# Kernel optimization log

Measured on AMD Instinct MI355X. Metric: run time of the kernel, lower is better.

The kernel has to match this reference:

```python
import jax, jax.numpy as jnp
import numpy as np

E = 1024
H = 16
D = E // H
NUM_BUCKETS = 320
MAX_DISTANCE = 800


def _relative_positions_bucket(relative_positions):
    # relative_positions: int32 [T, S]
    num_buckets = NUM_BUCKETS // 2  # 160
    relative_buckets = (relative_positions > 0).astype(jnp.int32) * num_buckets
    rel = jnp.abs(relative_positions)
    max_exact = num_buckets // 2  # 80
    is_small = rel < max_exact
    rel_f = jnp.maximum(rel, 1).astype(jnp.float32)
    large = jnp.log(rel_f / max_exact) / np.log(MAX_DISTANCE / max_exact) * (num_buckets - max_exact)
    large = (max_exact + large).astype(jnp.int32)
    large = jnp.minimum(large, num_buckets - 1)
    relative_buckets = relative_buckets + jnp.where(is_small, rel, large)
    return relative_buckets


def setup_inputs() -> dict:
    key = jax.random.key(0)
    ks = jax.random.split(key, 12)
    B, T = 2, 2048
    s = 0.02
    return {
        "hidden_states": jax.random.normal(ks[0], (B, T, E), dtype=jnp.float32),
        "q_w": jax.random.normal(ks[1], (E, E), dtype=jnp.float32) * s,
        "q_b": jnp.zeros((E,), dtype=jnp.float32),
        "k_w": jax.random.normal(ks[2], (E, E), dtype=jnp.float32) * s,
        "k_b": jnp.zeros((E,), dtype=jnp.float32),
        "v_w": jax.random.normal(ks[3], (E, E), dtype=jnp.float32) * s,
        "v_b": jnp.zeros((E,), dtype=jnp.float32),
        "out_w": jax.random.normal(ks[4], (E, E), dtype=jnp.float32) * s,
        "out_b": jnp.zeros((E,), dtype=jnp.float32),
        "rel_embed": jax.random.normal(ks[5], (NUM_BUCKETS, H), dtype=jnp.float32) * s,
        "gru_const": jnp.ones((1, H, 1, 1), dtype=jnp.float32),
        "gru_w": jax.random.normal(ks[6], (8, D), dtype=jnp.float32) * s,
        "gru_b": jnp.zeros((8,), dtype=jnp.float32),
    }


def reference(hidden_states, q_w, q_b, k_w, k_b, v_w, v_b, out_w, out_b,
              rel_embed, gru_const, gru_w, gru_b):
    B, T, _ = hidden_states.shape
    scaling = D ** (-0.5)

    # --- relative position bias: [H, T, T] ---
    ctx = jnp.arange(T, dtype=jnp.int32)[:, None]
    mem = jnp.arange(T, dtype=jnp.int32)[None, :]
    buckets = _relative_positions_bucket(mem - ctx)          # [T, T]
    position_bias = rel_embed[buckets]                        # [T, T, H]
    position_bias = jnp.transpose(position_bias, (2, 0, 1))   # [H, T, T]

    # --- gate (gru_rel_pos): per (b, h, t) scalar ---
    gated = hidden_states.reshape(B, T, H, D).transpose(0, 2, 1, 3)  # [B,H,T,D]
    proj = jnp.einsum('bhtd,ed->bhte', gated, gru_w) + gru_b         # [B,H,T,8]
    proj = proj.reshape(B, H, T, 2, 4).sum(-1)                        # [B,H,T,2]
    gate = jax.nn.sigmoid(proj)
    gate_a = gate[..., 0:1]
    gate_b = gate[..., 1:2]
    gate_out = gate_a * (gate_b * gru_const - 1.0) + 2.0              # [B,H,T,1]
    gated_position_bias = gate_out * position_bias[None]              # [B,H,T,T]

    # --- attention (same math as F.multi_head_attention_forward eager path) ---
    q = (hidden_states @ q_w.T + q_b).reshape(B, T, H, D).transpose(0, 2, 1, 3) * scaling
    k = (hidden_states @ k_w.T + k_b).reshape(B, T, H, D).transpose(0, 2, 1, 3)
    v = (hidden_states @ v_w.T + v_b).reshape(B, T, H, D).transpose(0, 2, 1, 3)

    scores = jnp.einsum('bhtd,bhsd->bhts', q, k) + gated_position_bias
    attn = jax.nn.softmax(scores, axis=-1)
    ctx_out = jnp.einsum('bhts,bhsd->bhtd', attn, v)                  # [B,H,T,D]
    ctx_out = ctx_out.transpose(0, 2, 1, 3).reshape(B, T, E)
    return ctx_out @ out_w.T + out_b
```

## Files before the change

kernel.cpp:

```cpp
#include <hip/hip_runtime.h>
#include <hip/hip_bf16.h>
#include <math.h>

typedef __bf16 bf16;
typedef __bf16 bf16x4 __attribute__((ext_vector_type(4)));
typedef __bf16 bf16x8 __attribute__((ext_vector_type(8)));
typedef float  f32x4  __attribute__((ext_vector_type(4)));

#define T_SEQ 2048
#define E_DIM 1024
#define H_NUM 16
#define D_DIM 64
#define NDELTA 4095
#define LOG2E 1.4426950408889634f

__device__ __forceinline__ void gld16(const bf16* g, bf16* l) {
  __builtin_amdgcn_global_load_lds((__attribute__((address_space(1))) void*)(g),
                                   (__attribute__((address_space(3))) void*)(l), 16, 0, 0);
}

__global__ void cast_bf16_kernel(const float* __restrict__ src, bf16* __restrict__ dst, int n4) {
  int i = blockIdx.x * blockDim.x + threadIdx.x;
  if (i >= n4) return;
  const float4 v = reinterpret_cast<const float4*>(src)[i];
  bf16x4 o;
  o[0] = (bf16)v.x; o[1] = (bf16)v.y; o[2] = (bf16)v.z; o[3] = (bf16)v.w;
  reinterpret_cast<bf16x4*>(dst)[i] = o;
}

__global__ void cast_w_kernel(const float* __restrict__ q_w, const float* __restrict__ k_w,
                              const float* __restrict__ v_w, const float* __restrict__ o_w,
                              bf16* __restrict__ wcat, bf16* __restrict__ wob) {
  int i = blockIdx.x * 256 + threadIdx.x;
  int sel = blockIdx.y;
  const float* src = (sel == 0) ? q_w : (sel == 1) ? k_w : (sel == 2) ? v_w : o_w;
  bf16* dst = (sel < 3) ? (wcat + (size_t)sel * 1048576) : wob;
  const float4 v = reinterpret_cast<const float4*>(src)[i];
  bf16x4 o;
  o[0] = (bf16)v.x; o[1] = (bf16)v.y; o[2] = (bf16)v.z; o[3] = (bf16)v.w;
  reinterpret_cast<bf16x4*>(dst)[i] = o;
}

__global__ void pb_kernel(const float* __restrict__ rel_embed, float* __restrict__ pbt) {
  int dd = blockIdx.x * 64 + threadIdx.x;
  if (dd >= NDELTA) return;
  int delta = dd - (T_SEQ - 1);
  int bucket = (delta > 0) ? 160 : 0;
  int rel = abs(delta);
  int v;
  if (rel < 80) {
    v = rel;
  } else {
    float rf = (float)(rel < 1 ? 1 : rel);
    float lf = logf(rf / 80.0f) * (80.0f / 2.302585092994046f);
    int lg = 80 + (int)lf;
    v = lg < 159 ? lg : 159;
  }
  bucket += v;
#pragma unroll
  for (int h = 0; h < H_NUM; h++)
    pbt[h * NDELTA + dd] = rel_embed[bucket * H_NUM + h];
}

__global__ __launch_bounds__(256)
void gate_kernel(const float* __restrict__ hs, const float* __restrict__ gru_w,
                 const float* __restrict__ gru_b, const float* __restrict__ gconst,
                 float* __restrict__ gate)
{
  __shared__ float w[512];
  int tid = threadIdx.x;
  w[tid] = gru_w[tid];
  w[tid + 256] = gru_w[tid + 256];
  __syncthreads();
  int idx = blockIdx.x * 256 + tid;
  int h  = idx & 15;
  int bt = idx >> 4;
  const float* x = hs + (size_t)bt * E_DIM + h * D_DIM;
  float acc[8] = {0,0,0,0,0,0,0,0};
  for (int d = 0; d < 64; d += 4) {
    float4 xv = *(const float4*)&x[d];
#pragma unroll
    for (int e = 0; e < 8; e++) {
      acc[e] += xv.x * w[e*64+d] + xv.y * w[e*64+d+1]
              + xv.z * w[e*64+d+2] + xv.w * w[e*64+d+3];
    }
  }
  float p0 = acc[0]+acc[1]+acc[2]+acc[3] + gru_b[0]+gru_b[1]+gru_b[2]+gru_b[3];
  float p1 = acc[4]+acc[5]+acc[6]+acc[7] + gru_b[4]+gru_b[5]+gru_b[6]+gru_b[7];
  float ga = 1.0f / (1.0f + expf(-p0));
  float gb = 1.0f / (1.0f + expf(-p1));
  float g = (ga * (gb * gconst[h] - 1.0f) + 2.0f) * LOG2E;
  int bb = bt >> 11;
  int t  = bt & (T_SEQ - 1);
  gate[((size_t)(bb * H_NUM + h)) * T_SEQ + t] = g;
}

template<int MODE, int BM, int BN>
__global__ __launch_bounds__(256, 4)
void gemm4_kernel(const bf16* __restrict__ A, const bf16* __restrict__ W,
                  const float* __restrict__ b0, const float* __restrict__ b1,
                  const float* __restrict__ b2, float qalpha,
                  void* __restrict__ out0, void* __restrict__ out1, void* __restrict__ out2)
{
  constexpr int AM = BM / 32;
  constexpr int AN = BN / 32;
  __shared__ bf16 As[2][BM * 32];
  __shared__ bf16 Bs[2][BN * 32];
  const int tid  = threadIdx.x;
  const int lane = tid & 63;
  const int wave = tid >> 6;
  const int m0 = blockIdx.y * BM;
  const int n0 = blockIdx.x * BN;
  const int wm = (wave >> 1) * (BM / 2);
  const int wn = (wave & 1) * (BN / 2);
  const int qd = lane >> 4;
  const int lm = lane & 15;

  const int row4 = lane >> 2;
  const int col8 = (lane & 3) * 8;
  const bf16* gA0 = A + (size_t)(m0 + wave * (BM / 4) + row4) * 1024 + col8;
  const bf16* gB0 = W + (size_t)(n0 + wave * (BN / 4) + row4) * 1024 + col8;
  bf16* lA = (bf16*)As + wave * (BM / 4) * 32;
  bf16* lB = (bf16*)Bs + wave * (BN / 4) * 32;

  gld16(gA0, lA);
  if (BM == 128) gld16(gA0 + (size_t)16 * 1024, lA + 512);
  gld16(gB0, lB);
  if (BN == 128) gld16(gB0 + (size_t)16 * 1024, lB + 512);
  __syncthreads();

  f32x4 acc[AM][AN] = {};

  for (int k0 = 0; k0 < 1024; k0 += 32) {
    const int buf = (k0 >> 5) & 1;
    if (k0 + 32 < 1024) {
      bf16* lA1 = lA + (buf ^ 1) * (BM * 32);
      bf16* lB1 = lB + (buf ^ 1) * (BN * 32);
      gld16(gA0 + k0 + 32, lA1);
      if (BM == 128) gld16(gA0 + (size_t)16 * 1024 + k0 + 32, lA1 + 512);
      gld16(gB0 + k0 + 32, lB1);
      if (BN == 128) gld16(gB0 + (size_t)16 * 1024 + k0 + 32, lB1 + 512);
    }
    bf16x8 af[AM], bfr[AN];
#pragma unroll
    for (int i = 0; i < AM; i++)
      af[i]  = *(const bf16x8*)&As[buf][(wm + i * 16 + lm) * 32 + qd * 8];
#pragma unroll
    for (int i = 0; i < AN; i++)
      bfr[i] = *(const bf16x8*)&Bs[buf][(wn + i * 16 + lm) * 32 + qd * 8];
#pragma unroll
    for (int im = 0; im < AM; im++)
#pragma unroll
      for (int in = 0; in < AN; in++)
        acc[im][in] = __builtin_amdgcn_mfma_f32_16x16x32_bf16(af[im], bfr[in], acc[im][in], 0, 0, 0);
    __syncthreads();
  }

  const int seg = n0 >> 10;
  const float* bias = (MODE == 0) ? b0 : (seg == 0 ? b0 : (seg == 1 ? b1 : b2));
  const float alpha = (MODE == 1 && seg == 0) ? qalpha : 1.0f;

#pragma unroll
  for (int im = 0; im < AM; im++) {
#pragma unroll
    for (int in = 0; in < AN; in++) {
      const int n  = n0 + wn + in * 16 + lm;
      const int n1 = n & 1023;
      const float bv = bias[n1];
      const int mb = m0 + wm + im * 16 + qd * 4;
      if (MODE == 0) {
        float* o = (float*)out0;
#pragma unroll
        for (int r = 0; r < 4; r++)
          o[(size_t)(mb + r) * 1024 + n1] = acc[im][in][r] + bv;
      } else if (seg == 2) {
        const int bb = mb >> 11;
        const int t  = mb & 2047;
        bf16x4 pk;
#pragma unroll
        for (int r = 0; r < 4; r++) pk[r] = (bf16)(acc[im][in][r] + bv);
        *(bf16x4*)&((bf16*)out2)[((size_t)(bb * 1024 + n1)) * 2048 + t] = pk;
      } else {
        bf16* o = (bf16*)(seg == 0 ? out0 : out1);
#pragma unroll
        for (int r = 0; r < 4; r++)
          o[(size_t)(mb + r) * 1024 + n1] = (bf16)((acc[im][in][r] + bv) * alpha);
      }
    }
  }
}

#define LK 72
__global__ __launch_bounds__(256)
void attn3_kernel(const bf16* __restrict__ Qg, const bf16* __restrict__ Kg,
                  const bf16* __restrict__ Vtg, const float* __restrict__ gate,
                  const float* __restrict__ pbt, bf16* __restrict__ ctx)
{
  __shared__ bf16 Ks[2][64 * LK];
  __shared__ bf16 Vs[2][64 * LK];
  __shared__ bf16 Ps[4][32 * LK];
  __shared__ float pbs[2176];

  const int t0 = blockIdx.x * 128;
  const int h  = blockIdx.y;
  const int b  = blockIdx.z;
  const int tid  = threadIdx.x;
  const int lane = tid & 63;
  const int wave = tid >> 6;
  const int qd = lane >> 4;
  const int lm = lane & 15;

  for (int i = tid; i < 2176; i += 256) {
    int idx = i - t0 + 1920;
    pbs[i] = (idx >= 0 && idx < NDELTA) ? pbt[h * NDELTA + idx] : 0.0f;
  }

  bf16x8 qf[2][2];
  float g[2];
#pragma unroll
  for (int nb = 0; nb < 2; nb++) {
    const int q = t0 + wave * 32 + nb * 16 + lm;
    const bf16* qrow = Qg + (size_t)(b * T_SEQ + q) * E_DIM + h * D_DIM;
    qf[nb][0] = *(const bf16x8*)(qrow + qd * 8);
    qf[nb][1] = *(const bf16x8*)(qrow + 32 + qd * 8);
    g[nb] = gate[((size_t)(b * H_NUM + h)) * T_SEQ + q];
  }

  const int srow = tid >> 2;
  const int scol = (tid & 3) * 16;
  const bf16* kgp = Kg  + ((size_t)(b * T_SEQ) + srow) * E_DIM + h * D_DIM + scol;
  const bf16* vgp = Vtg + ((size_t)(b * 1024) + h * D_DIM + srow) * T_SEQ + scol;

  {
    bf16x8 a0 = *(const bf16x8*)kgp;
    bf16x8 a1 = *(const bf16x8*)(kgp + 8);
    bf16x8 c0 = *(const bf16x8*)vgp;
    bf16x8 c1 = *(const bf16x8*)(vgp + 8);
    *(bf16x8*)&Ks[0][srow * LK + scol]     = a0;
    *(bf16x8*)&Ks[0][srow * LK + scol + 8] = a1;
    *(bf16x8*)&Vs[0][srow * LK + scol]     = c0;
    *(bf16x8*)&Vs[0][srow * LK + scol + 8] = c1;
  }
  __syncthreads();

  f32x4 o[4][2] = {};
  float li[2] = {0.0f, 0.0f};
  bf16* psw = &Ps[wave][0];

  for (int it = 0; it < T_SEQ / 64; it++) {
    const int s0 = it * 64;
    const int buf = it & 1;
    const bool more = (it + 1 < T_SEQ / 64);
    bf16x8 nk0, nk1, nv0, nv1;
    if (more) {
      const bf16* kn = kgp + (size_t)(s0 + 64) * E_DIM;
      const bf16* vn = vgp + (s0 + 64);
      nk0 = *(const bf16x8*)kn; nk1 = *(const bf16x8*)(kn + 8);
      nv0 = *(const bf16x8*)vn; nv1 = *(const bf16x8*)(vn + 8);
    }

    bf16x8 kf[4][2];
#pragma unroll
    for (int mb = 0; mb < 4; mb++) {
      kf[mb][0] = *(const bf16x8*)&Ks[buf][(16 * mb + lm) * LK + qd * 8];
      kf[mb][1] = *(const bf16x8*)&Ks[buf][(16 * mb + lm) * LK + 32 + qd * 8];
    }
#pragma unroll
    for (int nb = 0; nb < 2; nb++) {
      f32x4 sc[4];
#pragma unroll
      for (int mb = 0; mb < 4; mb++) {
        f32x4 t = {};
        t = __builtin_amdgcn_mfma_f32_16x16x32_bf16(kf[mb][0], qf[nb][0], t, 0, 0, 0);
        t = __builtin_amdgcn_mfma_f32_16x16x32_bf16(kf[mb][1], qf[nb][1], t, 0, 0, 0);
        sc[mb] = t;
      }
      const int ib = s0 + 4 * qd + 127 - (wave * 32 + nb * 16 + lm);
      float rs = 0.0f;
#pragma unroll
      for (int mb = 0; mb < 4; mb++) {
        bf16x4 pk;
#pragma unroll
        for (int r = 0; r < 4; r++) {
          float p = __builtin_amdgcn_exp2f(sc[mb][r] + g[nb] * pbs[ib + 16 * mb + r]);
          rs += p;
          pk[r] = (bf16)p;
        }
        *(bf16x4*)&psw[(nb * 16 + lm) * LK + 16 * mb + 4 * qd] = pk;
      }
      li[nb] += rs;
    }
    bf16x8 pf[2][2];
#pragma unroll
    for (int nb = 0; nb < 2; nb++) {
      pf[nb][0] = *(const bf16x8*)&psw[(nb * 16 + lm) * LK + qd * 8];
      pf[nb][1] = *(const bf16x8*)&psw[(nb * 16 + lm) * LK + 32 + qd * 8];
    }
#pragma unroll
    for (int db = 0; db < 4; db++) {
      bf16x8 vf0 = *(const bf16x8*)&Vs[buf][(16 * db + lm) * LK + qd * 8];
      bf16x8 vf1 = *(const bf16x8*)&Vs[buf][(16 * db + lm) * LK + 32 + qd * 8];
#pragma unroll
      for (int nb = 0; nb < 2; nb++) {
        o[db][nb] = __builtin_amdgcn_mfma_f32_16x16x32_bf16(vf0, pf[nb][0], o[db][nb], 0, 0, 0);
        o[db][nb] = __builtin_amdgcn_mfma_f32_16x16x32_bf16(vf1, pf[nb][1], o[db][nb], 0, 0, 0);
      }
    }
    if (more) {
      *(bf16x8*)&Ks[buf ^ 1][srow * LK + scol]     = nk0;
      *(bf16x8*)&Ks[buf ^ 1][srow * LK + scol + 8] = nk1;
      *(bf16x8*)&Vs[buf ^ 1][srow * LK + scol]     = nv0;
      *(bf16x8*)&Vs[buf ^ 1][srow * LK + scol + 8] = nv1;
    }
    __syncthreads();
  }

#pragma unroll
  for (int nb = 0; nb < 2; nb++) {
    li[nb] += __shfl_xor(li[nb], 16);
    li[nb] += __shfl_xor(li[nb], 32);
  }
#pragma unroll
  for (int nb = 0; nb < 2; nb++) {
    const float inv = 1.0f / li[nb];
    const int q = t0 + wave * 32 + nb * 16 + lm;
    bf16* obase = ctx + (size_t)(b * T_SEQ + q) * E_DIM + h * D_DIM + 4 * qd;
#pragma unroll
    for (int db = 0; db < 4; db++) {
      bf16x4 ov;
      ov[0] = (bf16)(o[db][nb][0] * inv); ov[1] = (bf16)(o[db][nb][1] * inv);
      ov[2] = (bf16)(o[db][nb][2] * inv); ov[3] = (bf16)(o[db][nb][3] * inv);
      *(bf16x4*)&obase[16 * db] = ov;
    }
  }
}

extern "C" void kernel_launch(void* const* d_in, const int* in_sizes, int n_in,
                              void* d_out, int out_size, void* d_ws, size_t ws_size,
                              hipStream_t stream)
{
  const float* hs     = (const float*)d_in[0];
  const float* q_w    = (const float*)d_in[1];
  const float* q_b    = (const float*)d_in[2];
  const float* k_w    = (const float*)d_in[3];
  const float* k_b    = (const float*)d_in[4];
  const float* v_w    = (const float*)d_in[5];
  const float* v_b    = (const float*)d_in[6];
  const float* out_w  = (const float*)d_in[7];
  const float* out_b  = (const float*)d_in[8];
  const float* rel    = (const float*)d_in[9];
  const float* gconst = (const float*)d_in[10];
  const float* gru_w  = (const float*)d_in[11];
  const float* gru_b  = (const float*)d_in[12];

  char* p = (char*)d_ws;
  bf16* hsb  = (bf16*)p; p += (size_t)4096 * 1024 * 2;
  bf16* wcat = (bf16*)p; p += (size_t)3072 * 1024 * 2;
  bf16* wob  = (bf16*)p; p += (size_t)1024 * 1024 * 2;
  bf16* Qb   = (bf16*)p; p += (size_t)4096 * 1024 * 2;
  bf16* Kb   = (bf16*)p; p += (size_t)4096 * 1024 * 2;
  bf16* Vtb  = (bf16*)p; p += (size_t)2048 * 2048 * 2;
  bf16* ctxb = (bf16*)p; p += (size_t)4096 * 1024 * 2;
  float* gatep = (float*)p; p += (size_t)2 * H_NUM * T_SEQ * 4;
  float* pbt   = (float*)p; p += (size_t)H_NUM * NDELTA * 4;

  cast_bf16_kernel<<<4096, 256, 0, stream>>>(hs, hsb, 1048576);
  cast_w_kernel<<<dim3(1024, 4), 256, 0, stream>>>(q_w, k_w, v_w, out_w, wcat, wob);
  pb_kernel<<<64, 64, 0, stream>>>(rel, pbt);
  gate_kernel<<<256, 256, 0, stream>>>(hs, gru_w, gru_b, gconst, gatep);

  const float qalpha = 0.125f * LOG2E;
  gemm4_kernel<1, 64, 128><<<dim3(24, 64), 256, 0, stream>>>(
      hsb, wcat, q_b, k_b, v_b, qalpha, Qb, Kb, Vtb);

  attn3_kernel<<<dim3(T_SEQ / 128, H_NUM, 2), 256, 0, stream>>>(Qb, Kb, Vtb, gatep, pbt, ctxb);

  gemm4_kernel<0, 64, 64><<<dim3(16, 64), 256, 0, stream>>>(
      ctxb, wob, out_b, nullptr, nullptr, 1.0f, d_out, nullptr, nullptr);
}
```

Baseline: 229.9 us.

## Read position bias from four shifted bf16 copies in global memory instead of LDS

The bias table is now built as four copies per head, each shifted by one element and stored in bf16, so that every lane can fetch its four consecutive bias values with a single aligned 8-byte load straight from global/L2. The per-block LDS staging of the bias and its scalar LDS reads inside the softmax loop are removed. This cuts LDS traffic and shared memory use, at the price of global loads in the inner loop and bf16 rounding of the bias values.

```diff
diff --git a/kernel.cpp b/kernel.cpp
--- a/kernel.cpp
+++ b/kernel.cpp
@@ -41,25 +41,30 @@
   reinterpret_cast<bf16x4*>(dst)[i] = o;
 }
 
-__global__ void pb_kernel(const float* __restrict__ rel_embed, float* __restrict__ pbt) {
-  int dd = blockIdx.x * 64 + threadIdx.x;
-  if (dd >= NDELTA) return;
-  int delta = dd - (T_SEQ - 1);
-  int bucket = (delta > 0) ? 160 : 0;
-  int rel = abs(delta);
-  int v;
-  if (rel < 80) {
-    v = rel;
-  } else {
-    float rf = (float)(rel < 1 ? 1 : rel);
-    float lf = logf(rf / 80.0f) * (80.0f / 2.302585092994046f);
-    int lg = 80 + (int)lf;
-    v = lg < 159 ? lg : 159;
-  }
-  bucket += v;
-#pragma unroll
-  for (int h = 0; h < H_NUM; h++)
-    pbt[h * NDELTA + dd] = rel_embed[bucket * H_NUM + h];
+__global__ void pbt4_kernel(const float* __restrict__ rel_embed, bf16* __restrict__ pbt4) {
+  int j = blockIdx.y * 256 + threadIdx.x;
+  int h = blockIdx.x;
+#pragma unroll
+  for (int c = 0; c < 4; c++) {
+    int idx = j + c;
+    float val = 0.0f;
+    if (idx < NDELTA) {
+      int delta = idx - 2047;
+      int bucket = (delta > 0) ? 160 : 0;
+      int rel = abs(delta);
+      int v;
+      if (rel < 80) {
+        v = rel;
+      } else {
+        float rf = (float)(rel < 1 ? 1 : rel);
+        float lf = logf(rf / 80.0f) * (80.0f / 2.302585092994046f);
+        int lg = 80 + (int)lf;
+        v = lg < 159 ? lg : 159;
+      }
+      val = rel_embed[(bucket + v) * H_NUM + h];
+    }
+    pbt4[((size_t)(h * 4 + c)) * 4096 + j] = (bf16)val;
+  }
 }
 
 __global__ __launch_bounds__(256)
@@ -192,14 +197,13 @@
 
 #define LK 72
 __global__ __launch_bounds__(256)
-void attn3_kernel(const bf16* __restrict__ Qg, const bf16* __restrict__ Kg,
+void attn7_kernel(const bf16* __restrict__ Qg, const bf16* __restrict__ Kg,
                   const bf16* __restrict__ Vtg, const float* __restrict__ gate,
-                  const float* __restrict__ pbt, bf16* __restrict__ ctx)
+                  const bf16* __restrict__ pbt4, bf16* __restrict__ ctx)
 {
   __shared__ bf16 Ks[2][64 * LK];
   __shared__ bf16 Vs[2][64 * LK];
   __shared__ bf16 Ps[4][32 * LK];
-  __shared__ float pbs[2176];
 
   const int t0 = blockIdx.x * 128;
   const int h  = blockIdx.y;
@@ -210,21 +214,21 @@
   const int qd = lane >> 4;
   const int lm = lane & 15;
 
-  for (int i = tid; i < 2176; i += 256) {
-    int idx = i - t0 + 1920;
-    pbs[i] = (idx >= 0 && idx < NDELTA) ? pbt[h * NDELTA + idx] : 0.0f;
-  }
-
   bf16x8 qf[2][2];
   float g[2];
+  int qn[2];
 #pragma unroll
   for (int nb = 0; nb < 2; nb++) {
     const int q = t0 + wave * 32 + nb * 16 + lm;
+    qn[nb] = q;
     const bf16* qrow = Qg + (size_t)(b * T_SEQ + q) * E_DIM + h * D_DIM;
     qf[nb][0] = *(const bf16x8*)(qrow + qd * 8);
     qf[nb][1] = *(const bf16x8*)(qrow + 32 + qd * 8);
     g[nb] = gate[((size_t)(b * H_NUM + h)) * T_SEQ + q];
   }
+
+  const int c = (3 - lm) & 3;
+  const bf16* pbp = pbt4 + ((size_t)(h * 4 + c)) * 4096;
 
   const int srow = tid >> 2;
   const int scol = (tid & 3) * 16;
@@ -259,6 +263,15 @@
       nv0 = *(const bf16x8*)vn; nv1 = *(const bf16x8*)(vn + 8);
     }
 
+    bf16x4 bb[2][4];
+#pragma unroll
+    for (int nb = 0; nb < 2; nb++) {
+      const int base = s0 + 4 * qd + 2047 - qn[nb] - c;
+#pragma unroll
+      for (int mb = 0; mb < 4; mb++)
+        bb[nb][mb] = *(const bf16x4*)&pbp[base + 16 * mb];
+    }
+
     bf16x8 kf[4][2];
 #pragma unroll
     for (int mb = 0; mb < 4; mb++) {
@@ -275,14 +288,13 @@
         t = __builtin_amdgcn_mfma_f32_16x16x32_bf16(kf[mb][1], qf[nb][1], t, 0, 0, 0);
         sc[mb] = t;
       }
-      const int ib = s0 + 4 * qd + 127 - (wave * 32 + nb * 16 + lm);
       float rs = 0.0f;
 #pragma unroll
       for (int mb = 0; mb < 4; mb++) {
         bf16x4 pk;
 #pragma unroll
         for (int r = 0; r < 4; r++) {
-          float p = __builtin_amdgcn_exp2f(sc[mb][r] + g[nb] * pbs[ib + 16 * mb + r]);
+          float p = __builtin_amdgcn_exp2f(sc[mb][r] + g[nb] * (float)bb[nb][mb][r]);
           rs += p;
           pk[r] = (bf16)p;
         }
@@ -323,7 +335,7 @@
 #pragma unroll
   for (int nb = 0; nb < 2; nb++) {
     const float inv = 1.0f / li[nb];
-    const int q = t0 + wave * 32 + nb * 16 + lm;
+    const int q = qn[nb];
     bf16* obase = ctx + (size_t)(b * T_SEQ + q) * E_DIM + h * D_DIM + 4 * qd;
 #pragma unroll
     for (int db = 0; db < 4; db++) {
@@ -362,18 +374,18 @@
   bf16* Vtb  = (bf16*)p; p += (size_t)2048 * 2048 * 2;
   bf16* ctxb = (bf16*)p; p += (size_t)4096 * 1024 * 2;
   float* gatep = (float*)p; p += (size_t)2 * H_NUM * T_SEQ * 4;
-  float* pbt   = (float*)p; p += (size_t)H_NUM * NDELTA * 4;
+  bf16* pbt4  = (bf16*)p; p += (size_t)H_NUM * 4 * 4096 * 2;
 
   cast_bf16_kernel<<<4096, 256, 0, stream>>>(hs, hsb, 1048576);
   cast_w_kernel<<<dim3(1024, 4), 256, 0, stream>>>(q_w, k_w, v_w, out_w, wcat, wob);
-  pb_kernel<<<64, 64, 0, stream>>>(rel, pbt);
+  pbt4_kernel<<<dim3(16, 16), 256, 0, stream>>>(rel, pbt4);
   gate_kernel<<<256, 256, 0, stream>>>(hs, gru_w, gru_b, gconst, gatep);
 
   const float qalpha = 0.125f * LOG2E;
   gemm4_kernel<1, 64, 128><<<dim3(24, 64), 256, 0, stream>>>(
       hsb, wcat, q_b, k_b, v_b, qalpha, Qb, Kb, Vtb);
 
-  attn3_kernel<<<dim3(T_SEQ / 128, H_NUM, 2), 256, 0, stream>>>(Qb, Kb, Vtb, gatep, pbt, ctxb);
+  attn7_kernel<<<dim3(T_SEQ / 128, H_NUM, 2), 256, 0, stream>>>(Qb, Kb, Vtb, gatep, pbt4, ctxb);
 
   gemm4_kernel<0, 64, 64><<<dim3(16, 64), 256, 0, stream>>>(
       ctxb, wob, out_b, nullptr, nullptr, 1.0f, d_out, nullptr, nullptr);
```

Result: slower. 255.5 us (+11.1%).
